# Performance work log

Hardware: AMD Instinct MI355X
Metric: run time of the kernel (lower is better)

## Reference

```python
import jax, jax.numpy as jnp
import numpy as np

NEG_INF = -1e9


def setup_inputs() -> dict:
    key0 = jax.random.key(0)
    ks = jax.random.split(key0, 7)
    B, Tq, Tv, D, U = 8, 512, 512, 512, 128
    query = jax.random.normal(ks[0], (B, Tq, D), dtype=jnp.float32)
    key = jax.random.normal(ks[1], (B, Tv, D), dtype=jnp.float32)
    value = jax.random.normal(ks[2], (B, Tv, D), dtype=jnp.float32)
    mask = jax.random.randint(ks[3], (B, Tv), 0, 2).astype(bool)
    mask = mask.at[:, 0].set(True)  # ensure no fully-masked row
    Wa = jax.random.normal(ks[4], (D, U), dtype=jnp.float32) * (1.0 / np.sqrt(D))
    Ua = jax.random.normal(ks[5], (D, U), dtype=jnp.float32) * (1.0 / np.sqrt(D))
    scale = jax.random.normal(ks[6], (U,), dtype=jnp.float32) * 0.1
    return {"query": query, "key": key, "value": value, "mask": mask,
            "Wa": Wa, "Ua": Ua, "scale": scale}


def reference(query, key, value, mask, Wa, Ua, scale):
    # Dense projections (no bias)
    q = query @ Wa          # [B, Tq, U]
    k = key @ Ua            # [B, Tv, U]
    # Additive (Bahdanau) scores with learned per-unit scale:
    # scores[b,i,j] = sum_u scale[u] * tanh(q[b,i,u] + k[b,j,u])
    t = jnp.tanh(q[:, :, None, :] + k[:, None, :, :])   # [B, Tq, Tv, U]
    scores = jnp.einsum('bijU,U->bij', t, scale)         # [B, Tq, Tv]
    # Mask padded keys/values then softmax over Tv
    scores = jnp.where(mask[:, None, :], scores, NEG_INF)
    weights = jax.nn.softmax(scores, axis=-1)            # [B, Tq, Tv]
    # Weighted sum of values (query_mask is all-True in source -> no-op)
    context = jnp.einsum('bij,bjd->bid', weights, value) # [B, Tq, D]
    return context
```

## Files before the change

kernel.cpp:

```cpp
#include <hip/hip_runtime.h>

constexpr int Bb = 8;
constexpr int Tq = 512;
constexpr int Tv = 512;
constexpr int Dd = 512;
constexpr int Uu = 128;
constexpr float C2LOG2E = 2.88539008177792681f;

__global__ __launch_bounds__(512, 8) void proj_kernel(
    const float* __restrict__ query,
    const float* __restrict__ key,
    const float* __restrict__ Wa,
    const float* __restrict__ Ua,
    const int* __restrict__ mask,
    float* __restrict__ qf2, float* __restrict__ kT,
    int* __restrict__ jl_g, int* __restrict__ cnt_g)
{
    const int R    = blockIdx.x * 8;
    const bool isQ = R < Bb * Tq;
    const float* __restrict__ src = isQ ? query : key;
    const float* __restrict__ W   = isQ ? Wa : Ua;
    const int Rloc = isQ ? R : R - Bb * Tq;

    __shared__ float smem[8 * 8 * 128];
    __shared__ int posLoc[8];
    float* __restrict__ x = smem;
    const int t = threadIdx.x;

    {
        const float4* __restrict__ s4 =
            reinterpret_cast<const float4*>(src + (size_t)Rloc * Dd);
        float4* x4 = reinterpret_cast<float4*>(x);
#pragma unroll
        for (int m = 0; m < 2; ++m) x4[t + 512 * m] = s4[t + 512 * m];
    }
    if (!isQ && t < 64) {
        const int b  = Rloc >> 9;
        const int j0 = Rloc & 511;
        const bool writer = (j0 == 0);
        int base = 0;
#pragma unroll
        for (int c = 0; c < 8; ++c) {
            const int j = c * 64 + t;
            const int v = (mask[b * 512 + j] != 0);
            const unsigned long long bits = __ballot(v);
            const int pos = base + (int)__popcll(bits & ((1ull << t) - 1ull));
            if (j >= j0 && j < j0 + 8) posLoc[j - j0] = v ? pos : -1;
            if (writer && v) jl_g[b * 512 + pos] = j;
            base += (int)__popcll(bits);
        }
        if (writer && t == 0) cnt_g[b] = base;
    }
    __syncthreads();

    const int ub = t & 63;
    const int dq = t >> 6;
    const float* __restrict__ Wq = W + (size_t)dq * 64 * Uu;
    const float* __restrict__ xq = x + dq * 64;

    float acc[8][2];
#pragma unroll
    for (int r = 0; r < 8; ++r) { acc[r][0] = 0.f; acc[r][1] = 0.f; }

#pragma unroll 2
    for (int d4 = 0; d4 < 16; ++d4) {
        const int d = d4 * 4;
        const float w0x = Wq[(d + 0) * Uu + ub], w1x = Wq[(d + 0) * Uu + ub + 64];
        const float w0y = Wq[(d + 1) * Uu + ub], w1y = Wq[(d + 1) * Uu + ub + 64];
        const float w0z = Wq[(d + 2) * Uu + ub], w1z = Wq[(d + 2) * Uu + ub + 64];
        const float w0w = Wq[(d + 3) * Uu + ub], w1w = Wq[(d + 3) * Uu + ub + 64];
#pragma unroll
        for (int r = 0; r < 8; ++r) {
            const float4 xv = *reinterpret_cast<const float4*>(xq + r * Dd + d);
            acc[r][0] = fmaf(xv.x, w0x, acc[r][0]);
            acc[r][0] = fmaf(xv.y, w0y, acc[r][0]);
            acc[r][0] = fmaf(xv.z, w0z, acc[r][0]);
            acc[r][0] = fmaf(xv.w, w0w, acc[r][0]);
            acc[r][1] = fmaf(xv.x, w1x, acc[r][1]);
            acc[r][1] = fmaf(xv.y, w1y, acc[r][1]);
            acc[r][1] = fmaf(xv.z, w1z, acc[r][1]);
            acc[r][1] = fmaf(xv.w, w1w, acc[r][1]);
        }
    }

    __syncthreads();
    {
        float* __restrict__ part = smem;
#pragma unroll
        for (int r = 0; r < 8; ++r) {
            part[(dq * 8 + r) * 128 + ub]      = acc[r][0];
            part[(dq * 8 + r) * 128 + ub + 64] = acc[r][1];
        }
    }
    __syncthreads();

    {
        const float* __restrict__ part = smem;
        const int r  = t >> 6;
        const int u0 = (t & 63) * 2;
        float s0 = 0.f, s1 = 0.f;
#pragma unroll
        for (int p = 0; p < 8; ++p) {
            const float2 pv = *reinterpret_cast<const float2*>(part + (p * 8 + r) * 128 + u0);
            s0 += pv.x;
            s1 += pv.y;
        }
        float2 e;
        e.x = __builtin_amdgcn_exp2f(C2LOG2E * s0);
        e.y = __builtin_amdgcn_exp2f(C2LOG2E * s1);
        if (isQ) {
            *reinterpret_cast<float2*>(qf2 + (size_t)(Rloc + r) * Uu + u0) = e;
        } else {
            const int p = posLoc[r];
            if (p >= 0) {
                float* __restrict__ kb = kT + (size_t)(Rloc >> 9) * Uu * Tv;
                const int u4 = u0 >> 2;
                const int c  = u0 & 3;
                *reinterpret_cast<float2*>(kb + ((size_t)u4 * Tv + p) * 4 + c) = e;
            }
        }
    }
}

__global__ __launch_bounds__(512, 8) void attn_kernel(
    const float* __restrict__ qf2, const float* __restrict__ kT,
    const float* __restrict__ value,
    const int* __restrict__ jl_g, const int* __restrict__ cnt_g,
    const float* __restrict__ scale,
    float* __restrict__ out)
{
    const int bid = blockIdx.x;
    const int swz = (bid & 7) * 128 + (bid >> 3);
    const int r0 = swz * 4;
    const int b  = r0 >> 9;
    const int t  = threadIdx.x;

    __shared__ float q2[4 * Uu];
    __shared__ float s2[Uu];
    __shared__ int   jl[Tv];
    __shared__ float w[4 * Tv];
    __shared__ float pbuf[4 * Tv];
    __shared__ float sums8[8];
    const int cnt = cnt_g[b];

    if (t < 128)
        reinterpret_cast<float4*>(q2)[t] =
            reinterpret_cast<const float4*>(qf2 + (size_t)r0 * Uu)[t];
    else if (t < 160)
        reinterpret_cast<float4*>(s2)[t - 128] =
            reinterpret_cast<const float4*>(scale)[t - 128];
    jl[t] = (t < cnt) ? jl_g[b * 512 + t] : 0;
    __syncthreads();

    const int cntp4 = (cnt + 3) & ~3;

    {
        const int g   = t >> 8;
        const int jc0 = t & 255;
        const float4* __restrict__ kb4 =
            reinterpret_cast<const float4*>(kT) + (size_t)b * 32 * Tv + (size_t)g * 16 * Tv;
        float* __restrict__ wr = g ? pbuf : w;
        for (int jb = 0; jb < cnt; jb += 256) {
            const int jc = jb + jc0;
            if (jc < cnt) {
                float acc[4] = {0, 0, 0, 0};
#pragma unroll 4
                for (int u4 = 0; u4 < 16; ++u4) {
                    const float4 kv = kb4[(size_t)u4 * Tv + jc];
                    const float4 sv = reinterpret_cast<const float4*>(s2)[g * 16 + u4];
#pragma unroll
                    for (int i = 0; i < 4; ++i) {
                        const float4 qv = *reinterpret_cast<const float4*>(
                            q2 + i * Uu + (g * 16 + u4) * 4);
                        const float pa = fmaf(qv.x, kv.x, 1.f);
                        const float pb = fmaf(qv.y, kv.y, 1.f);
                        const float pc = fmaf(qv.z, kv.z, 1.f);
                        const float pd = fmaf(qv.w, kv.w, 1.f);
                        const float ra = __builtin_amdgcn_rcpf(pa * pb);
                        const float rc = __builtin_amdgcn_rcpf(pc * pd);
                        acc[i] = fmaf(sv.x, ra * pb, acc[i]);
                        acc[i] = fmaf(sv.y, ra * pa, acc[i]);
                        acc[i] = fmaf(sv.z, rc * pd, acc[i]);
                        acc[i] = fmaf(sv.w, rc * pc, acc[i]);
                    }
                }
#pragma unroll
                for (int i = 0; i < 4; ++i) wr[i * Tv + jc] = acc[i];
            }
        }
    }
    __syncthreads();

    {
        const int wv = t >> 6, ln = t & 63;
        const int i = wv >> 1, h = wv & 1;
        float* __restrict__ row        = w    + i * Tv;
        const float* __restrict__ rowB = pbuf + i * Tv;
        float sum = 0.f;
#pragma unroll
        for (int c = 0; c < 4; ++c) {
            const int e = ln + 64 * (h * 4 + c);
            if (e < cnt) {
                const float ex = __builtin_amdgcn_exp2f(-C2LOG2E * (row[e] + rowB[e]));
                row[e] = ex;
                sum += ex;
            } else {
                row[e] = 0.f;
            }
        }
#pragma unroll
        for (int off = 32; off; off >>= 1) sum += __shfl_xor(sum, off, 64);
        if (ln == 0) sums8[wv] = sum;
    }
    __syncthreads();

    const int mid = ((cntp4 >> 1) + 3) & ~3;
    const int g  = t >> 8;
    const int c  = t & 255;
    const int d0 = c * 2;
    const int jbeg = g ? mid : 0;
    const int jend = g ? cntp4 : mid;
    const float* __restrict__ vb = value + (size_t)b * Tv * Dd + d0;
    float ax[4], ay[4];
#pragma unroll
    for (int i = 0; i < 4; ++i) { ax[i] = 0.f; ay[i] = 0.f; }

    if (jbeg < jend) {
        int jj = jbeg;
        int4 rows = *reinterpret_cast<const int4*>(jl + jj);
        float2 v0 = *reinterpret_cast<const float2*>(vb + (size_t)rows.x * Dd);
        float2 v1 = *reinterpret_cast<const float2*>(vb + (size_t)rows.y * Dd);
        float2 v2 = *reinterpret_cast<const float2*>(vb + (size_t)rows.z * Dd);
        float2 v3 = *reinterpret_cast<const float2*>(vb + (size_t)rows.w * Dd);
        for (; jj + 4 < jend; jj += 4) {
            const int4 rowsN = *reinterpret_cast<const int4*>(jl + jj + 4);
            const float2 n0 = *reinterpret_cast<const float2*>(vb + (size_t)rowsN.x * Dd);
            const float2 n1 = *reinterpret_cast<const float2*>(vb + (size_t)rowsN.y * Dd);
            const float2 n2 = *reinterpret_cast<const float2*>(vb + (size_t)rowsN.z * Dd);
            const float2 n3 = *reinterpret_cast<const float2*>(vb + (size_t)rowsN.w * Dd);
#pragma unroll
            for (int i = 0; i < 4; ++i) {
                const float4 wq = *reinterpret_cast<const float4*>(w + i * Tv + jj);
                ax[i] = fmaf(wq.x, v0.x, ax[i]); ay[i] = fmaf(wq.x, v0.y, ay[i]);
                ax[i] = fmaf(wq.y, v1.x, ax[i]); ay[i] = fmaf(wq.y, v1.y, ay[i]);
                ax[i] = fmaf(wq.z, v2.x, ax[i]); ay[i] = fmaf(wq.z, v2.y, ay[i]);
                ax[i] = fmaf(wq.w, v3.x, ax[i]); ay[i] = fmaf(wq.w, v3.y, ay[i]);
            }
            v0 = n0; v1 = n1; v2 = n2; v3 = n3;
        }
#pragma unroll
        for (int i = 0; i < 4; ++i) {
            const float4 wq = *reinterpret_cast<const float4*>(w + i * Tv + jj);
            ax[i] = fmaf(wq.x, v0.x, ax[i]); ay[i] = fmaf(wq.x, v0.y, ay[i]);
            ax[i] = fmaf(wq.y, v1.x, ax[i]); ay[i] = fmaf(wq.y, v1.y, ay[i]);
            ax[i] = fmaf(wq.z, v2.x, ax[i]); ay[i] = fmaf(wq.z, v2.y, ay[i]);
            ax[i] = fmaf(wq.w, v3.x, ax[i]); ay[i] = fmaf(wq.w, v3.y, ay[i]);
        }
    }

    if (g == 1) {
#pragma unroll
        for (int i = 0; i < 4; ++i) {
            float2 p; p.x = ax[i]; p.y = ay[i];
            *reinterpret_cast<float2*>(pbuf + i * Dd + d0) = p;
        }
    }
    __syncthreads();
    if (g == 0) {
#pragma unroll
        for (int i = 0; i < 4; ++i) {
            const float inv = 1.0f / (sums8[2 * i] + sums8[2 * i + 1]);
            const float2 p1 = *reinterpret_cast<const float2*>(pbuf + i * Dd + d0);
            float2 o;
            o.x = (ax[i] + p1.x) * inv;
            o.y = (ay[i] + p1.y) * inv;
            *reinterpret_cast<float2*>(out + (size_t)(r0 + i) * Dd + d0) = o;
        }
    }
}

extern "C" void kernel_launch(void* const* d_in, const int* in_sizes, int n_in,
                              void* d_out, int out_size, void* d_ws, size_t ws_size,
                              hipStream_t stream)
{
    const float* query = (const float*)d_in[0];
    const float* key   = (const float*)d_in[1];
    const float* value = (const float*)d_in[2];
    const int*   mask  = (const int*)d_in[3];
    const float* Wa    = (const float*)d_in[4];
    const float* Ua    = (const float*)d_in[5];
    const float* scale = (const float*)d_in[6];
    float* out = (float*)d_out;

    float* qf2 = (float*)d_ws;
    float* kT  = qf2 + Bb * Tq * Uu;
    int*   jl_g  = (int*)(kT + Bb * Uu * Tv);
    int*   cnt_g = jl_g + Bb * Tv;

    proj_kernel<<<(2 * Bb * Tq) / 8, 512, 0, stream>>>(query, key, Wa, Ua, mask,
                                                       qf2, kT, jl_g, cnt_g);
    attn_kernel<<<(Bb * Tq) / 4, 512, 0, stream>>>(qf2, kT, value, jl_g, cnt_g,
                                                   scale, out);
}
```

Measured before the change: 150.9 us.

## Drop LDS staging and split attention PV reduction four ways with float4 columns

The projection kernel now reads input rows straight from global memory instead of staging them in shared memory, and loads weights as float2. This removes two block barriers. The attention kernel likewise reads q and scale directly from global memory, removing an initial barrier. The weighted-value accumulation is now split across four wave groups over key positions, each handling float4 columns, then reduced through a larger shared buffer. This drops the explicit software prefetch of value rows and raises shared memory use, which may reduce occupancy.

```diff
diff --git a/kernel.cpp b/kernel.cpp
--- a/kernel.cpp
+++ b/kernel.cpp
@@ -22,18 +22,10 @@
     const float* __restrict__ W   = isQ ? Wa : Ua;
     const int Rloc = isQ ? R : R - Bb * Tq;
 
-    __shared__ float smem[8 * 8 * 128];
+    __shared__ float part[8 * 8 * 128];
     __shared__ int posLoc[8];
-    float* __restrict__ x = smem;
     const int t = threadIdx.x;
 
-    {
-        const float4* __restrict__ s4 =
-            reinterpret_cast<const float4*>(src + (size_t)Rloc * Dd);
-        float4* x4 = reinterpret_cast<float4*>(x);
-#pragma unroll
-        for (int m = 0; m < 2; ++m) x4[t + 512 * m] = s4[t + 512 * m];
-    }
     if (!isQ && t < 64) {
         const int b  = Rloc >> 9;
         const int j0 = Rloc & 511;
@@ -51,12 +43,11 @@
         }
         if (writer && t == 0) cnt_g[b] = base;
     }
-    __syncthreads();
-
-    const int ub = t & 63;
-    const int dq = t >> 6;
+
+    const int u2 = (t & 63) * 2;
+    const int dq = __builtin_amdgcn_readfirstlane(t >> 6);
     const float* __restrict__ Wq = W + (size_t)dq * 64 * Uu;
-    const float* __restrict__ xq = x + dq * 64;
+    const float* __restrict__ xs = src + (size_t)Rloc * Dd + dq * 64;
 
     float acc[8][2];
 #pragma unroll
@@ -65,37 +56,34 @@
 #pragma unroll 2
     for (int d4 = 0; d4 < 16; ++d4) {
         const int d = d4 * 4;
-        const float w0x = Wq[(d + 0) * Uu + ub], w1x = Wq[(d + 0) * Uu + ub + 64];
-        const float w0y = Wq[(d + 1) * Uu + ub], w1y = Wq[(d + 1) * Uu + ub + 64];
-        const float w0z = Wq[(d + 2) * Uu + ub], w1z = Wq[(d + 2) * Uu + ub + 64];
-        const float w0w = Wq[(d + 3) * Uu + ub], w1w = Wq[(d + 3) * Uu + ub + 64];
+        const float2 w0 = *reinterpret_cast<const float2*>(Wq + (d + 0) * Uu + u2);
+        const float2 w1 = *reinterpret_cast<const float2*>(Wq + (d + 1) * Uu + u2);
+        const float2 w2 = *reinterpret_cast<const float2*>(Wq + (d + 2) * Uu + u2);
+        const float2 w3 = *reinterpret_cast<const float2*>(Wq + (d + 3) * Uu + u2);
 #pragma unroll
         for (int r = 0; r < 8; ++r) {
-            const float4 xv = *reinterpret_cast<const float4*>(xq + r * Dd + d);
-            acc[r][0] = fmaf(xv.x, w0x, acc[r][0]);
-            acc[r][0] = fmaf(xv.y, w0y, acc[r][0]);
-            acc[r][0] = fmaf(xv.z, w0z, acc[r][0]);
-            acc[r][0] = fmaf(xv.w, w0w, acc[r][0]);
-            acc[r][1] = fmaf(xv.x, w1x, acc[r][1]);
-            acc[r][1] = fmaf(xv.y, w1y, acc[r][1]);
-            acc[r][1] = fmaf(xv.z, w1z, acc[r][1]);
-            acc[r][1] = fmaf(xv.w, w1w, acc[r][1]);
-        }
-    }
-
-    __syncthreads();
-    {
-        float* __restrict__ part = smem;
+            const float4 xv = *reinterpret_cast<const float4*>(xs + r * Dd + d);
+            acc[r][0] = fmaf(xv.x, w0.x, acc[r][0]);
+            acc[r][1] = fmaf(xv.x, w0.y, acc[r][1]);
+            acc[r][0] = fmaf(xv.y, w1.x, acc[r][0]);
+            acc[r][1] = fmaf(xv.y, w1.y, acc[r][1]);
+            acc[r][0] = fmaf(xv.z, w2.x, acc[r][0]);
+            acc[r][1] = fmaf(xv.z, w2.y, acc[r][1]);
+            acc[r][0] = fmaf(xv.w, w3.x, acc[r][0]);
+            acc[r][1] = fmaf(xv.w, w3.y, acc[r][1]);
+        }
+    }
+
+    {
 #pragma unroll
         for (int r = 0; r < 8; ++r) {
-            part[(dq * 8 + r) * 128 + ub]      = acc[r][0];
-            part[(dq * 8 + r) * 128 + ub + 64] = acc[r][1];
-        }
-    }
-    __syncthreads();
-
-    {
-        const float* __restrict__ part = smem;
+            float2 p; p.x = acc[r][0]; p.y = acc[r][1];
+            *reinterpret_cast<float2*>(part + (dq * 8 + r) * 128 + u2) = p;
+        }
+    }
+    __syncthreads();
+
+    {
         const int r  = t >> 6;
         const int u0 = (t & 63) * 2;
         float s0 = 0.f, s1 = 0.f;
@@ -135,28 +123,22 @@
     const int b  = r0 >> 9;
     const int t  = threadIdx.x;
 
-    __shared__ float q2[4 * Uu];
-    __shared__ float s2[Uu];
     __shared__ int   jl[Tv];
     __shared__ float w[4 * Tv];
-    __shared__ float pbuf[4 * Tv];
+    __shared__ float pbuf[12 * Dd];
     __shared__ float sums8[8];
+
     const int cnt = cnt_g[b];
-
-    if (t < 128)
-        reinterpret_cast<float4*>(q2)[t] =
-            reinterpret_cast<const float4*>(qf2 + (size_t)r0 * Uu)[t];
-    else if (t < 160)
-        reinterpret_cast<float4*>(s2)[t - 128] =
-            reinterpret_cast<const float4*>(scale)[t - 128];
     jl[t] = (t < cnt) ? jl_g[b * 512 + t] : 0;
-    __syncthreads();
-
+
+    const int wvu = __builtin_amdgcn_readfirstlane(t >> 6);
     const int cntp4 = (cnt + 3) & ~3;
 
     {
-        const int g   = t >> 8;
+        const int g   = wvu >> 2;
         const int jc0 = t & 255;
+        const float* __restrict__ qs = qf2 + (size_t)r0 * Uu + g * 64;
+        const float* __restrict__ ss = scale + g * 64;
         const float4* __restrict__ kb4 =
             reinterpret_cast<const float4*>(kT) + (size_t)b * 32 * Tv + (size_t)g * 16 * Tv;
         float* __restrict__ wr = g ? pbuf : w;
@@ -167,11 +149,11 @@
 #pragma unroll 4
                 for (int u4 = 0; u4 < 16; ++u4) {
                     const float4 kv = kb4[(size_t)u4 * Tv + jc];
-                    const float4 sv = reinterpret_cast<const float4*>(s2)[g * 16 + u4];
+                    const float4 sv = *reinterpret_cast<const float4*>(ss + u4 * 4);
 #pragma unroll
                     for (int i = 0; i < 4; ++i) {
                         const float4 qv = *reinterpret_cast<const float4*>(
-                            q2 + i * Uu + (g * 16 + u4) * 4);
+                            qs + i * Uu + u4 * 4);
                         const float pa = fmaf(qv.x, kv.x, 1.f);
                         const float pb = fmaf(qv.y, kv.y, 1.f);
                         const float pc = fmaf(qv.z, kv.z, 1.f);
@@ -192,8 +174,8 @@
     __syncthreads();
 
     {
-        const int wv = t >> 6, ln = t & 63;
-        const int i = wv >> 1, h = wv & 1;
+        const int ln = t & 63;
+        const int i = wvu >> 1, h = wvu & 1;
         float* __restrict__ row        = w    + i * Tv;
         const float* __restrict__ rowB = pbuf + i * Tv;
         float sum = 0.f;
@@ -210,71 +192,61 @@
         }
 #pragma unroll
         for (int off = 32; off; off >>= 1) sum += __shfl_xor(sum, off, 64);
-        if (ln == 0) sums8[wv] = sum;
-    }
-    __syncthreads();
-
-    const int mid = ((cntp4 >> 1) + 3) & ~3;
-    const int g  = t >> 8;
-    const int c  = t & 255;
-    const int d0 = c * 2;
-    const int jbeg = g ? mid : 0;
-    const int jend = g ? cntp4 : mid;
+        if (ln == 0) sums8[wvu] = sum;
+    }
+    __syncthreads();
+
+    const int g2 = wvu >> 1;
+    const int cc = t & 127;
+    const int d0 = cc * 4;
+    const int chunk = ((cntp4 + 15) >> 4) << 2;
+    const int jbeg = g2 * chunk;
+    const int jend = min(jbeg + chunk, cntp4);
     const float* __restrict__ vb = value + (size_t)b * Tv * Dd + d0;
-    float ax[4], ay[4];
-#pragma unroll
-    for (int i = 0; i < 4; ++i) { ax[i] = 0.f; ay[i] = 0.f; }
-
-    if (jbeg < jend) {
-        int jj = jbeg;
-        int4 rows = *reinterpret_cast<const int4*>(jl + jj);
-        float2 v0 = *reinterpret_cast<const float2*>(vb + (size_t)rows.x * Dd);
-        float2 v1 = *reinterpret_cast<const float2*>(vb + (size_t)rows.y * Dd);
-        float2 v2 = *reinterpret_cast<const float2*>(vb + (size_t)rows.z * Dd);
-        float2 v3 = *reinterpret_cast<const float2*>(vb + (size_t)rows.w * Dd);
-        for (; jj + 4 < jend; jj += 4) {
-            const int4 rowsN = *reinterpret_cast<const int4*>(jl + jj + 4);
-            const float2 n0 = *reinterpret_cast<const float2*>(vb + (size_t)rowsN.x * Dd);
-            const float2 n1 = *reinterpret_cast<const float2*>(vb + (size_t)rowsN.y * Dd);
-            const float2 n2 = *reinterpret_cast<const float2*>(vb + (size_t)rowsN.z * Dd);
-            const float2 n3 = *reinterpret_cast<const float2*>(vb + (size_t)rowsN.w * Dd);
-#pragma unroll
-            for (int i = 0; i < 4; ++i) {
-                const float4 wq = *reinterpret_cast<const float4*>(w + i * Tv + jj);
-                ax[i] = fmaf(wq.x, v0.x, ax[i]); ay[i] = fmaf(wq.x, v0.y, ay[i]);
-                ax[i] = fmaf(wq.y, v1.x, ax[i]); ay[i] = fmaf(wq.y, v1.y, ay[i]);
-                ax[i] = fmaf(wq.z, v2.x, ax[i]); ay[i] = fmaf(wq.z, v2.y, ay[i]);
-                ax[i] = fmaf(wq.w, v3.x, ax[i]); ay[i] = fmaf(wq.w, v3.y, ay[i]);
-            }
-            v0 = n0; v1 = n1; v2 = n2; v3 = n3;
-        }
+    float4 ax[4];
+#pragma unroll
+    for (int i = 0; i < 4; ++i) ax[i] = make_float4(0.f, 0.f, 0.f, 0.f);
+
+#pragma unroll 2
+    for (int jj = jbeg; jj < jend; jj += 4) {
+        const int4 rows = *reinterpret_cast<const int4*>(jl + jj);
+        const float4 v0 = *reinterpret_cast<const float4*>(vb + (size_t)rows.x * Dd);
+        const float4 v1 = *reinterpret_cast<const float4*>(vb + (size_t)rows.y * Dd);
+        const float4 v2 = *reinterpret_cast<const float4*>(vb + (size_t)rows.z * Dd);
+        const float4 v3 = *reinterpret_cast<const float4*>(vb + (size_t)rows.w * Dd);
 #pragma unroll
         for (int i = 0; i < 4; ++i) {
             const float4 wq = *reinterpret_cast<const float4*>(w + i * Tv + jj);
-            ax[i] = fmaf(wq.x, v0.x, ax[i]); ay[i] = fmaf(wq.x, v0.y, ay[i]);
-            ax[i] = fmaf(wq.y, v1.x, ax[i]); ay[i] = fmaf(wq.y, v1.y, ay[i]);
-            ax[i] = fmaf(wq.z, v2.x, ax[i]); ay[i] = fmaf(wq.z, v2.y, ay[i]);
-            ax[i] = fmaf(wq.w, v3.x, ax[i]); ay[i] = fmaf(wq.w, v3.y, ay[i]);
-        }
-    }
-
-    if (g == 1) {
-#pragma unroll
-        for (int i = 0; i < 4; ++i) {
-            float2 p; p.x = ax[i]; p.y = ay[i];
-            *reinterpret_cast<float2*>(pbuf + i * Dd + d0) = p;
-        }
-    }
-    __syncthreads();
-    if (g == 0) {
+            ax[i].x = fmaf(wq.x, v0.x, ax[i].x); ax[i].y = fmaf(wq.x, v0.y, ax[i].y);
+            ax[i].z = fmaf(wq.x, v0.z, ax[i].z); ax[i].w = fmaf(wq.x, v0.w, ax[i].w);
+            ax[i].x = fmaf(wq.y, v1.x, ax[i].x); ax[i].y = fmaf(wq.y, v1.y, ax[i].y);
+            ax[i].z = fmaf(wq.y, v1.z, ax[i].z); ax[i].w = fmaf(wq.y, v1.w, ax[i].w);
+            ax[i].x = fmaf(wq.z, v2.x, ax[i].x); ax[i].y = fmaf(wq.z, v2.y, ax[i].y);
+            ax[i].z = fmaf(wq.z, v2.z, ax[i].z); ax[i].w = fmaf(wq.z, v2.w, ax[i].w);
+            ax[i].x = fmaf(wq.w, v3.x, ax[i].x); ax[i].y = fmaf(wq.w, v3.y, ax[i].y);
+            ax[i].z = fmaf(wq.w, v3.z, ax[i].z); ax[i].w = fmaf(wq.w, v3.w, ax[i].w);
+        }
+    }
+
+    if (g2 != 0) {
+#pragma unroll
+        for (int i = 0; i < 4; ++i)
+            *reinterpret_cast<float4*>(pbuf + ((size_t)(g2 - 1) * 4 + i) * Dd + d0) = ax[i];
+    }
+    __syncthreads();
+    if (g2 == 0) {
 #pragma unroll
         for (int i = 0; i < 4; ++i) {
             const float inv = 1.0f / (sums8[2 * i] + sums8[2 * i + 1]);
-            const float2 p1 = *reinterpret_cast<const float2*>(pbuf + i * Dd + d0);
-            float2 o;
-            o.x = (ax[i] + p1.x) * inv;
-            o.y = (ay[i] + p1.y) * inv;
-            *reinterpret_cast<float2*>(out + (size_t)(r0 + i) * Dd + d0) = o;
+            const float4 p1 = *reinterpret_cast<const float4*>(pbuf + ((size_t)0 * 4 + i) * Dd + d0);
+            const float4 p2 = *reinterpret_cast<const float4*>(pbuf + ((size_t)1 * 4 + i) * Dd + d0);
+            const float4 p3 = *reinterpret_cast<const float4*>(pbuf + ((size_t)2 * 4 + i) * Dd + d0);
+            float4 o;
+            o.x = (ax[i].x + p1.x + p2.x + p3.x) * inv;
+            o.y = (ax[i].y + p1.y + p2.y + p3.y) * inv;
+            o.z = (ax[i].z + p1.z + p2.z + p3.z) * inv;
+            o.w = (ax[i].w + p1.w + p2.w + p3.w) * inv;
+            *reinterpret_cast<float4*>(out + (size_t)(r0 + i) * Dd + d0) = o;
         }
     }
 }
```

Result: no change. 151.2 us (+0.2%).
